# Performance work log

Measured on AMD Instinct MI355X. Metric: run time of the kernel, lower is better.

## Reference

```python
import jax, jax.numpy as jnp
import numpy as np

N_SCALES = 3
BASE_SIGMA = 0.1
SCALES = jnp.asarray([BASE_SIGMA * 2.0 ** i for i in range(N_SCALES)], dtype=jnp.float32)


def setup_inputs() -> dict:
    key = jax.random.key(0)
    k_x, k_pos, k_tp, k_w1, k_b1, k_w2, k_b2 = jax.random.split(key, 7)
    B, C, T = 16, 306, 4000
    M = 128
    x = jax.random.normal(k_x, (B, C, T), dtype=jnp.float32)
    positions = jax.random.normal(k_pos, (B, C, 2), dtype=jnp.float32)
    target_positions = jax.random.normal(k_tp, (M, 2), dtype=jnp.float32)
    # nn.Linear(3, 32) / nn.Linear(32, 1) params (kaiming-uniform-ish init)
    lim1 = 1.0 / np.sqrt(3.0)
    w1 = jax.random.uniform(k_w1, (3, 32), jnp.float32, -lim1, lim1)
    b1 = jax.random.uniform(k_b1, (32,), jnp.float32, -lim1, lim1)
    lim2 = 1.0 / np.sqrt(32.0)
    w2 = jax.random.uniform(k_w2, (32, 1), jnp.float32, -lim2, lim2)
    b2 = jax.random.uniform(k_b2, (1,), jnp.float32, -lim2, lim2)
    return {"x": x, "positions": positions, "target_positions": target_positions,
            "w1": w1, "b1": b1, "w2": w2, "b2": b2}


def reference(x, positions, target_positions, w1, b1, w2, b2):
    # squared euclidean distances [B, C, M]
    diff = positions[:, :, None, :] - target_positions[None, None, :, :]
    d2 = jnp.sum(diff * diff, axis=-1)
    # multi-scale Gaussian kernels, stacked on last axis -> [B, C, M, n_scales]
    inv = 1.0 / (2.0 * SCALES ** 2)  # [n_scales]
    scale_weights = jnp.exp(-d2[..., None] * inv)
    # tiny 2-layer MLP gate: (3 -> 32 -> 1)
    h = jax.nn.relu(scale_weights @ w1 + b1)  # [B, C, M, 32]
    w = (h @ w2 + b2)[..., 0]                 # [B, C, M]
    # normalize over channel dim
    w = w / (jnp.sum(w, axis=1, keepdims=True) + 1e-8)
    # weighted channel aggregation -> [B, M, T]
    return jnp.einsum('bct,bcm->bmt', x, w)
```

## Files before the change

kernel.cpp:

```cpp
#include <hip/hip_runtime.h>

#define B_ 16
#define C_ 306
#define CP_ 320
#define T_ 4000
#define M_ 128

typedef short bf16x8 __attribute__((ext_vector_type(8)));
typedef float f32x4 __attribute__((ext_vector_type(4)));

__global__ __launch_bounds__(320)
void gate_kernel(const float* __restrict__ positions,
                 const float* __restrict__ target,
                 const float* __restrict__ w1,
                 const float* __restrict__ b1,
                 const float* __restrict__ w2,
                 const float* __restrict__ b2,
                 unsigned short* __restrict__ w_hi,
                 unsigned short* __restrict__ w_lo,
                 float* __restrict__ scale) {
    const int bm = blockIdx.x;
    const int b = bm >> 7;
    const int m = bm & (M_ - 1);
    const int tid = threadIdx.x;

    __shared__ float s_w1[96], s_b1[32], s_w2[32];
    __shared__ float s_b2, s_tx, s_ty;
    __shared__ float s_part[5];

    if (tid < 96) s_w1[tid] = w1[tid];
    if (tid < 32) { s_b1[tid] = b1[tid]; s_w2[tid] = w2[tid]; }
    if (tid == 256) s_b2 = b2[0];
    if (tid == 257) s_tx = target[m * 2 + 0];
    if (tid == 258) s_ty = target[m * 2 + 1];
    __syncthreads();

    float w = 0.0f;
    if (tid < C_) {
        const float px = positions[(b * C_ + tid) * 2 + 0];
        const float py = positions[(b * C_ + tid) * 2 + 1];
        const float dx = px - s_tx, dy = py - s_ty;
        const float d2 = dx * dx + dy * dy;
        const float s0 = __expf(-d2 * 50.0f);
        const float s1 = __expf(-d2 * 12.5f);
        const float s2 = __expf(-d2 * 3.125f);
        float acc = s_b2;
#pragma unroll
        for (int j = 0; j < 32; ++j) {
            float h = fmaf(s0, s_w1[j],
                      fmaf(s1, s_w1[32 + j],
                      fmaf(s2, s_w1[64 + j], s_b1[j])));
            acc = fmaf(fmaxf(h, 0.0f), s_w2[j], acc);
        }
        w = acc;
    }

    float s = w;
#pragma unroll
    for (int off = 32; off > 0; off >>= 1) s += __shfl_down(s, off, 64);
    if ((tid & 63) == 0) s_part[tid >> 6] = s;
    __syncthreads();
    if (tid == 0) {
        float tot = s_part[0] + s_part[1] + s_part[2] + s_part[3] + s_part[4];
        scale[bm] = 1.0f / (tot + 1e-8f);
    }

    const unsigned int u = __float_as_uint(w);
    const unsigned short h = (unsigned short)(u >> 16);
    const float lof = w - __uint_as_float(u & 0xffff0000u);
    const unsigned short l = (unsigned short)(__float_as_uint(lof) >> 16);
    w_hi[(size_t)bm * CP_ + tid] = h;
    w_lo[(size_t)bm * CP_ + tid] = l;
}

__global__ __launch_bounds__(256, 2)
void merge_gemm(const float* __restrict__ x,
                const unsigned short* __restrict__ w_hi,
                const unsigned short* __restrict__ w_lo,
                const float* __restrict__ scale,
                float* __restrict__ out) {
    const int t0 = blockIdx.x * 128;
    const int b  = blockIdx.y;
    const int tid  = threadIdx.x;
    const int lane = tid & 63;
    const int wv   = tid >> 6;
    const int tquad = lane >> 4;
    const int tsub  = lane & 15;

    __shared__ __align__(16) unsigned short sWh[4096];
    __shared__ __align__(16) unsigned short sWl[4096];
    __shared__ __align__(16) unsigned short sXh[4096];
    __shared__ __align__(16) unsigned short sXl[4096];
    __shared__ __align__(16) float sScale[M_];

    if (tid < M_) sScale[tid] = scale[b * M_ + tid];

    const float* xb = x + (size_t)b * C_ * T_;
    const unsigned short* whB = w_hi + (size_t)b * M_ * CP_;
    const unsigned short* wlB = w_lo + (size_t)b * M_ * CP_;

    f32x4 acc[4][4];
#pragma unroll
    for (int i = 0; i < 4; ++i)
#pragma unroll
        for (int j = 0; j < 4; ++j) acc[i][j] = (f32x4){0.f, 0.f, 0.f, 0.f};

    const int mw = (wv & 1) * 64;
    const int tw = (wv >> 1) * 64;

    for (int step = 0; step < CP_ / 32; ++step) {
        const int c0 = step * 32;

#pragma unroll
        for (int pp = 0; pp < 2; ++pp) {
            const int idx = tid + 256 * pp;
            const int mm = idx >> 2;
            const int r  = idx & 3;
            const size_t goff = (size_t)mm * CP_ + c0 + r * 8;
            *(uint4*)(sWh + (r * 128 + mm) * 8) = *(const uint4*)(whB + goff);
            *(uint4*)(sWl + (r * 128 + mm) * 8) = *(const uint4*)(wlB + goff);
        }

#pragma unroll
        for (int s = 0; s < 2; ++s) {
            const int t = wv * 16 + tsub + s * 64;
            const int tg = min(t0 + t, T_ - 1);
            const float* xcol = xb + tg;
#pragma unroll
            for (int k = 0; k < 4; ++k) {
                const int p = tquad + 4 * k;
                const int c = c0 + 2 * p;
                const int ca = min(c, C_ - 1);
                const int cb = min(c + 1, C_ - 1);
                const float xa = xcol[(size_t)ca * T_];
                const float xv = xcol[(size_t)cb * T_];
                const unsigned int ua = __float_as_uint(xa);
                const unsigned int ub = __float_as_uint(xv);
                const unsigned int hp = (ua >> 16) | (ub & 0xffff0000u);
                const float la = xa - __uint_as_float(ua & 0xffff0000u);
                const float lb = xv - __uint_as_float(ub & 0xffff0000u);
                const unsigned int lp = (__float_as_uint(la) >> 16) |
                                        (__float_as_uint(lb) & 0xffff0000u);
                const int off32 = (p >> 2) * 512 + t * 4 + (p & 3);
                ((unsigned int*)sXh)[off32] = hp;
                ((unsigned int*)sXl)[off32] = lp;
            }
        }
        __syncthreads();

        bf16x8 ah[4], al[4], bh[4], bl[4];
#pragma unroll
        for (int i = 0; i < 4; ++i) {
            const int moff = tquad * 1024 + (mw + i * 16 + tsub) * 8;
            ah[i] = *(const bf16x8*)(sWh + moff);
            al[i] = *(const bf16x8*)(sWl + moff);
            const int toff = tquad * 1024 + (tw + i * 16 + tsub) * 8;
            bh[i] = *(const bf16x8*)(sXh + toff);
            bl[i] = *(const bf16x8*)(sXl + toff);
        }
#pragma unroll
        for (int mi = 0; mi < 4; ++mi)
#pragma unroll
            for (int ti = 0; ti < 4; ++ti) {
                acc[mi][ti] = __builtin_amdgcn_mfma_f32_16x16x32_bf16(
                    ah[mi], bh[ti], acc[mi][ti], 0, 0, 0);
                acc[mi][ti] = __builtin_amdgcn_mfma_f32_16x16x32_bf16(
                    ah[mi], bl[ti], acc[mi][ti], 0, 0, 0);
                acc[mi][ti] = __builtin_amdgcn_mfma_f32_16x16x32_bf16(
                    al[mi], bh[ti], acc[mi][ti], 0, 0, 0);
            }
        __syncthreads();
    }

#pragma unroll
    for (int mi = 0; mi < 4; ++mi) {
        const int mbase = mw + mi * 16 + tquad * 4;
        const float4 sc = *(const float4*)(sScale + mbase);
#pragma unroll
        for (int ti = 0; ti < 4; ++ti) {
            const int tg = t0 + tw + ti * 16 + tsub;
            if (tg < T_) {
                float* op = out + ((size_t)b * M_ + mbase) * T_ + tg;
                op[0 * T_] = acc[mi][ti][0] * sc.x;
                op[1 * T_] = acc[mi][ti][1] * sc.y;
                op[2 * T_] = acc[mi][ti][2] * sc.z;
                op[3 * T_] = acc[mi][ti][3] * sc.w;
            }
        }
    }
}

extern "C" void kernel_launch(void* const* d_in, const int* in_sizes, int n_in,
                              void* d_out, int out_size, void* d_ws, size_t ws_size,
                              hipStream_t stream) {
    const float* x         = (const float*)d_in[0];
    const float* positions = (const float*)d_in[1];
    const float* target    = (const float*)d_in[2];
    const float* w1        = (const float*)d_in[3];
    const float* b1        = (const float*)d_in[4];
    const float* w2        = (const float*)d_in[5];
    const float* b2        = (const float*)d_in[6];
    float* out = (float*)d_out;

    unsigned short* w_hi = (unsigned short*)d_ws;
    unsigned short* w_lo = w_hi + (size_t)B_ * M_ * CP_;
    float* scale = (float*)(w_lo + (size_t)B_ * M_ * CP_);

    gate_kernel<<<B_ * M_, 320, 0, stream>>>(positions, target, w1, b1, w2, b2,
                                             w_hi, w_lo, scale);

    dim3 grid((T_ + 127) / 128, B_);
    merge_gemm<<<grid, 256, 0, stream>>>(x, w_hi, w_lo, scale, out);
}
```

Before: 150.0 us.

## Batch gate targets per block, load W fragments from global, widen K step

The gate kernel now computes 4 targets per block with positions staged in shared memory. It derives the three Gaussian scales from one exp by repeated squaring instead of three exps. The GEMM drops the shared-memory staging of the W hi/lo tiles, reading the A fragments straight from global (L2-resident) memory. It also processes 64 channels per sync step and raises the occupancy hint to 3 blocks per CU. The aim is fewer barriers and less LDS traffic, at the risk of global-load latency on the A operand and more register pressure.

Measured after the change: 151.4 us. About the same (+0.9%).

```diff
diff --git a/kernel.cpp b/kernel.cpp
--- a/kernel.cpp
+++ b/kernel.cpp
@@ -19,61 +19,71 @@
                  unsigned short* __restrict__ w_hi,
                  unsigned short* __restrict__ w_lo,
                  float* __restrict__ scale) {
-    const int bm = blockIdx.x;
-    const int b = bm >> 7;
-    const int m = bm & (M_ - 1);
+    const int b  = blockIdx.x >> 5;
+    const int mg = blockIdx.x & 31;
     const int tid = threadIdx.x;
 
     __shared__ float s_w1[96], s_b1[32], s_w2[32];
-    __shared__ float s_b2, s_tx, s_ty;
+    __shared__ float2 s_pos[C_];
+    __shared__ float s_b2;
+    __shared__ float s_tgt[8];
     __shared__ float s_part[5];
 
     if (tid < 96) s_w1[tid] = w1[tid];
     if (tid < 32) { s_b1[tid] = b1[tid]; s_w2[tid] = w2[tid]; }
     if (tid == 256) s_b2 = b2[0];
-    if (tid == 257) s_tx = target[m * 2 + 0];
-    if (tid == 258) s_ty = target[m * 2 + 1];
+    if (tid < C_) s_pos[tid] = ((const float2*)positions)[b * C_ + tid];
+    if (tid >= 312) s_tgt[tid - 312] = target[mg * 8 + (tid - 312)];
     __syncthreads();
 
-    float w = 0.0f;
-    if (tid < C_) {
-        const float px = positions[(b * C_ + tid) * 2 + 0];
-        const float py = positions[(b * C_ + tid) * 2 + 1];
-        const float dx = px - s_tx, dy = py - s_ty;
-        const float d2 = dx * dx + dy * dy;
-        const float s0 = __expf(-d2 * 50.0f);
-        const float s1 = __expf(-d2 * 12.5f);
-        const float s2 = __expf(-d2 * 3.125f);
-        float acc = s_b2;
-#pragma unroll
-        for (int j = 0; j < 32; ++j) {
-            float h = fmaf(s0, s_w1[j],
-                      fmaf(s1, s_w1[32 + j],
-                      fmaf(s2, s_w1[64 + j], s_b1[j])));
-            acc = fmaf(fmaxf(h, 0.0f), s_w2[j], acc);
-        }
-        w = acc;
+    float px = 0.0f, py = 0.0f;
+    if (tid < C_) { px = s_pos[tid].x; py = s_pos[tid].y; }
+
+#pragma unroll
+    for (int mi = 0; mi < 4; ++mi) {
+        float w = 0.0f;
+        if (tid < C_) {
+            const float dx = px - s_tgt[mi * 2 + 0];
+            const float dy = py - s_tgt[mi * 2 + 1];
+            const float d2 = dx * dx + dy * dy;
+            const float s2 = __expf(-d2 * 3.125f);
+            const float q  = s2 * s2;
+            const float s1 = q * q;
+            const float r  = s1 * s1;
+            const float s0 = r * r;
+            float acc = s_b2;
+#pragma unroll
+            for (int j = 0; j < 32; ++j) {
+                float h = fmaf(s0, s_w1[j],
+                          fmaf(s1, s_w1[32 + j],
+                          fmaf(s2, s_w1[64 + j], s_b1[j])));
+                acc = fmaf(fmaxf(h, 0.0f), s_w2[j], acc);
+            }
+            w = acc;
+        }
+
+        float s = w;
+#pragma unroll
+        for (int off = 32; off > 0; off >>= 1) s += __shfl_down(s, off, 64);
+        if ((tid & 63) == 0) s_part[tid >> 6] = s;
+        __syncthreads();
+        if (tid == 0) {
+            float tot = s_part[0] + s_part[1] + s_part[2] + s_part[3] + s_part[4];
+            scale[b * M_ + mg * 4 + mi] = 1.0f / (tot + 1e-8f);
+        }
+        __syncthreads();
+
+        const unsigned int u = __float_as_uint(w);
+        const unsigned short h = (unsigned short)(u >> 16);
+        const float lof = w - __uint_as_float(u & 0xffff0000u);
+        const unsigned short l = (unsigned short)(__float_as_uint(lof) >> 16);
+        const size_t off = (size_t)(b * M_ + mg * 4 + mi) * CP_ + tid;
+        w_hi[off] = h;
+        w_lo[off] = l;
     }
-
-    float s = w;
-#pragma unroll
-    for (int off = 32; off > 0; off >>= 1) s += __shfl_down(s, off, 64);
-    if ((tid & 63) == 0) s_part[tid >> 6] = s;
-    __syncthreads();
-    if (tid == 0) {
-        float tot = s_part[0] + s_part[1] + s_part[2] + s_part[3] + s_part[4];
-        scale[bm] = 1.0f / (tot + 1e-8f);
-    }
-
-    const unsigned int u = __float_as_uint(w);
-    const unsigned short h = (unsigned short)(u >> 16);
-    const float lof = w - __uint_as_float(u & 0xffff0000u);
-    const unsigned short l = (unsigned short)(__float_as_uint(lof) >> 16);
-    w_hi[(size_t)bm * CP_ + tid] = h;
-    w_lo[(size_t)bm * CP_ + tid] = l;
 }
 
-__global__ __launch_bounds__(256, 2)
+__global__ __launch_bounds__(256, 3)
 void merge_gemm(const float* __restrict__ x,
                 const unsigned short* __restrict__ w_hi,
                 const unsigned short* __restrict__ w_lo,
@@ -87,10 +97,8 @@
     const int tquad = lane >> 4;
     const int tsub  = lane & 15;
 
-    __shared__ __align__(16) unsigned short sWh[4096];
-    __shared__ __align__(16) unsigned short sWl[4096];
-    __shared__ __align__(16) unsigned short sXh[4096];
-    __shared__ __align__(16) unsigned short sXl[4096];
+    __shared__ __align__(16) unsigned short sXh[8192];
+    __shared__ __align__(16) unsigned short sXl[8192];
     __shared__ __align__(16) float sScale[M_];
 
     if (tid < M_) sScale[tid] = scale[b * M_ + tid];
@@ -108,18 +116,8 @@
     const int mw = (wv & 1) * 64;
     const int tw = (wv >> 1) * 64;
 
-    for (int step = 0; step < CP_ / 32; ++step) {
-        const int c0 = step * 32;
-
-#pragma unroll
-        for (int pp = 0; pp < 2; ++pp) {
-            const int idx = tid + 256 * pp;
-            const int mm = idx >> 2;
-            const int r  = idx & 3;
-            const size_t goff = (size_t)mm * CP_ + c0 + r * 8;
-            *(uint4*)(sWh + (r * 128 + mm) * 8) = *(const uint4*)(whB + goff);
-            *(uint4*)(sWl + (r * 128 + mm) * 8) = *(const uint4*)(wlB + goff);
-        }
+    for (int step = 0; step < CP_ / 64; ++step) {
+        const int c0 = step * 64;
 
 #pragma unroll
         for (int s = 0; s < 2; ++s) {
@@ -127,7 +125,7 @@
             const int tg = min(t0 + t, T_ - 1);
             const float* xcol = xb + tg;
 #pragma unroll
-            for (int k = 0; k < 4; ++k) {
+            for (int k = 0; k < 8; ++k) {
                 const int p = tquad + 4 * k;
                 const int c = c0 + 2 * p;
                 const int ca = min(c, C_ - 1);
@@ -148,27 +146,33 @@
         }
         __syncthreads();
 
-        bf16x8 ah[4], al[4], bh[4], bl[4];
-#pragma unroll
-        for (int i = 0; i < 4; ++i) {
-            const int moff = tquad * 1024 + (mw + i * 16 + tsub) * 8;
-            ah[i] = *(const bf16x8*)(sWh + moff);
-            al[i] = *(const bf16x8*)(sWl + moff);
-            const int toff = tquad * 1024 + (tw + i * 16 + tsub) * 8;
-            bh[i] = *(const bf16x8*)(sXh + toff);
-            bl[i] = *(const bf16x8*)(sXl + toff);
-        }
-#pragma unroll
-        for (int mi = 0; mi < 4; ++mi)
-#pragma unroll
-            for (int ti = 0; ti < 4; ++ti) {
-                acc[mi][ti] = __builtin_amdgcn_mfma_f32_16x16x32_bf16(
-                    ah[mi], bh[ti], acc[mi][ti], 0, 0, 0);
-                acc[mi][ti] = __builtin_amdgcn_mfma_f32_16x16x32_bf16(
-                    ah[mi], bl[ti], acc[mi][ti], 0, 0, 0);
-                acc[mi][ti] = __builtin_amdgcn_mfma_f32_16x16x32_bf16(
-                    al[mi], bh[ti], acc[mi][ti], 0, 0, 0);
-            }
+#pragma unroll
+        for (int ks = 0; ks < 2; ++ks) {
+            const int cb0 = c0 + ks * 32;
+
+            bf16x8 bh[4], bl[4];
+#pragma unroll
+            for (int i = 0; i < 4; ++i) {
+                const int toff = ((ks * 4 + tquad) * 128 + tw + i * 16 + tsub) * 8;
+                bh[i] = *(const bf16x8*)(sXh + toff);
+                bl[i] = *(const bf16x8*)(sXl + toff);
+            }
+#pragma unroll
+            for (int mi = 0; mi < 4; ++mi) {
+                const size_t woff = (size_t)(mw + mi * 16 + tsub) * CP_ + cb0 + tquad * 8;
+                const bf16x8 ah = *(const bf16x8*)(whB + woff);
+                const bf16x8 al = *(const bf16x8*)(wlB + woff);
+#pragma unroll
+                for (int ti = 0; ti < 4; ++ti) {
+                    acc[mi][ti] = __builtin_amdgcn_mfma_f32_16x16x32_bf16(
+                        ah, bh[ti], acc[mi][ti], 0, 0, 0);
+                    acc[mi][ti] = __builtin_amdgcn_mfma_f32_16x16x32_bf16(
+                        ah, bl[ti], acc[mi][ti], 0, 0, 0);
+                    acc[mi][ti] = __builtin_amdgcn_mfma_f32_16x16x32_bf16(
+                        al, bh[ti], acc[mi][ti], 0, 0, 0);
+                }
+            }
+        }
         __syncthreads();
     }
 
@@ -206,7 +210,7 @@
     unsigned short* w_lo = w_hi + (size_t)B_ * M_ * CP_;
     float* scale = (float*)(w_lo + (size_t)B_ * M_ * CP_);
 
-    gate_kernel<<<B_ * M_, 320, 0, stream>>>(positions, target, w1, b1, w2, b2,
+    gate_kernel<<<B_ * 32, 320, 0, stream>>>(positions, target, w1, b1, w2, b2,
                                              w_hi, w_lo, scale);
 
     dim3 grid((T_ + 127) / 128, B_);
```
